# Kernel tuning notes

Hardware: AMD Instinct MI355X
Metric: run time of the kernel (lower is better)

The kernel has to match this reference:

```python
import jax, jax.numpy as jnp
import numpy as np

BETA = 0.25


def setup_inputs() -> dict:
    key = jax.random.key(0)
    k1, k2 = jax.random.split(key)
    z_e = jax.random.normal(k1, (16, 64, 64, 64), dtype=jnp.float32)  # (B, D, H, W)
    embedding = jax.random.normal(k2, (1024, 64), dtype=jnp.float32)  # (K, D)
    return {"z_e": z_e, "embedding": embedding}


def reference(z_e, embedding):
    B, D, H, W = z_e.shape
    # (B, D, H, W) -> (B, H, W, D) -> (N, D)
    flat = jnp.transpose(z_e, (0, 2, 3, 1)).reshape(-1, D)
    # squared L2 distances to codebook: (N, K)
    dist = (jnp.sum(flat * flat, axis=1, keepdims=True)
            + jnp.sum(embedding * embedding, axis=1)
            - 2.0 * flat @ embedding.T)
    indices = jnp.argmin(dist, axis=1)  # (N,)
    z_q_flat = embedding[indices]  # (N, D) gather
    z_q = jnp.transpose(z_q_flat.reshape(B, H, W, D), (0, 3, 1, 2))  # (B, D, H, W)
    codebook_loss = jnp.mean((jax.lax.stop_gradient(z_q) - z_e) ** 2)
    commit_loss = jnp.mean((z_q - jax.lax.stop_gradient(z_e)) ** 2)
    vq_loss = codebook_loss + BETA * commit_loss
    # straight-through estimator
    z_q_st = z_e + jax.lax.stop_gradient(z_q - z_e)
    return (z_q_st, vq_loss, indices.reshape(B, H, W))
```

## Files before the change

### kernel.cpp

```cpp
#include <hip/hip_runtime.h>
#include <math.h>

typedef short  short8 __attribute__((ext_vector_type(8)));
typedef float  f32x4  __attribute__((ext_vector_type(4)));

#define ZQ_ELEMS 4194304
#define KC       1024
#define EPS_HALF 0.005f


__device__ inline unsigned short bf16_rne(float f) {
    union { float fv; unsigned u; } a; a.fv = f;
    unsigned r = a.u + 0x7FFFu + ((a.u >> 16) & 1u);
    return (unsigned short)(r >> 16);
}
__device__ inline float bf16_to_f(unsigned short h) {
    union { unsigned u; float fv; } a; a.u = ((unsigned)h) << 16;
    return a.fv;
}
__device__ inline double dpack(float hi, unsigned lo) {
    return __hiloint2double(__float_as_int(hi), (int)lo);
}
__device__ inline float dhi(double d) { return __int_as_float(__double2hiint(d)); }
__device__ inline unsigned dlo(double d) { return (unsigned)__double2loint(d); }

__global__ __launch_bounds__(256) void vq_prep(const float* __restrict__ emb,
        unsigned short* __restrict__ epack, float* __restrict__ enorm,
        int* __restrict__ risky_cnt, float* __restrict__ out) {
    const int k = blockIdx.x * 256 + threadIdx.x;
    if (k == 0) { *risky_cnt = 0; out[ZQ_ELEMS] = 0.f; }
    const float4* e4 = (const float4*)(emb + k * 64);
    float s = 0.f;
#pragma unroll
    for (int j = 0; j < 16; ++j) {
        float4 v = e4[j];
        float vv[4] = {v.x, v.y, v.z, v.w};
        ushort4 hv, lv;
        unsigned short h[4], l[4];
#pragma unroll
        for (int t = 0; t < 4; ++t) {
            s = fmaf(vv[t], vv[t], s);
            h[t] = bf16_rne(vv[t]);
            l[t] = bf16_rne(vv[t] - bf16_to_f(h[t]));
        }
        hv.x = h[0]; hv.y = h[1]; hv.z = h[2]; hv.w = h[3];
        lv.x = l[0]; lv.y = l[1]; lv.z = l[2]; lv.w = l[3];
        *(ushort4*)(epack + k * 128 + j * 4)      = hv;
        *(ushort4*)(epack + k * 128 + 64 + j * 4) = lv;
    }
    enorm[k] = s;
}

__global__ __launch_bounds__(256) void vq_scan(const float* __restrict__ z_e,
        const unsigned short* __restrict__ epack, const float* __restrict__ enorm,
        const float* __restrict__ emb, float* __restrict__ out,
        int* __restrict__ risky_cnt, int* __restrict__ risky) {
    const int tid  = threadIdx.x;
    const int lane = tid & 63;
    const int col  = lane & 15;
    const int g    = lane >> 4;
    const int wv   = __builtin_amdgcn_readfirstlane(tid >> 6);
    const int pblk = blockIdx.x * 64;

    __shared__ __align__(16) char smem[19456];
    unsigned short* afrag = (unsigned short*)smem;
    double* mrgB = (double*)(smem + 16384);
    float*  mrgS = (float*)(smem + 18432);
    float (*zq)[65] = (float (*)[65])smem;
    __shared__ int   sidx[64];
    __shared__ float sred[4];

    {
        const int lp = tid & 63;
        const int pg = pblk + lp;
        const float* zb = z_e + (pg >> 12) * 262144 + (pg & 4095);
        const int sx = (lp & 7) << 3;
#pragma unroll
        for (int s8 = 0; s8 < 2; ++s8) {
            const int d0 = wv * 16 + s8 * 8;
            short8 H, L;
#pragma unroll
            for (int j = 0; j < 8; ++j) {
                float v = zb[(d0 + j) * 4096];
                unsigned short h = bf16_rne(v);
                H[j] = (short)h;
                L[j] = (short)bf16_rne(v - bf16_to_f(h));
            }
            const int sw = d0 ^ sx;
            *(short8*)&afrag[lp * 128 + sw]      = H;
            *(short8*)&afrag[lp * 128 + 64 + sw] = L;
        }
    }
    __syncthreads();

    const f32x4 zero4 = {0.f, 0.f, 0.f, 0.f};
    const int g8 = g * 8;

    double Brun[4];
    float  Srun[4];
#pragma unroll
    for (int it = 0; it < 4; ++it) { Brun[it] = dpack(-INFINITY, 0u); Srun[it] = -INFINITY; }

#pragma unroll 1
    for (int pass = 0; pass < 4; ++pass) {
        const int cbase = pass * 256 + wv * 64;
        short8 ah[4][2], al[4][2];
        f32x4 enf[4];
#pragma unroll
        for (int t = 0; t < 4; ++t) {
            const int code = cbase + t * 16 + col;
            const short8* ph = (const short8*)(epack + code * 128) + g;
            ah[t][0] = ph[0]; ah[t][1] = ph[4];
            al[t][0] = ph[8]; al[t][1] = ph[12];
            const float4 e4 = *(const float4*)(enorm + cbase + t * 16 + g * 4);
            enf[t][0] = -0.5f * e4.x; enf[t][1] = -0.5f * e4.y;
            enf[t][2] = -0.5f * e4.z; enf[t][3] = -0.5f * e4.w;
        }
        const int K1 = 1023 - cbase - g * 4;

#pragma unroll
        for (int it = 0; it < 4; ++it) {
            const int lpx = it * 16 + col;
            const int sxp = (lpx & 7) << 3;
            const unsigned short* ap = &afrag[lpx * 128];
            const short8 bh0 = *(const short8*)&ap[(g8     ) ^ sxp];
            const short8 bh1 = *(const short8*)&ap[(32 + g8) ^ sxp];
            const short8 bl0 = *(const short8*)&ap[64 + ((g8     ) ^ sxp)];
            const short8 bl1 = *(const short8*)&ap[64 + ((32 + g8) ^ sxp)];

            double cand[16];
#pragma unroll
            for (int t = 0; t < 4; ++t) {
                f32x4 aA, aB;
                aA = __builtin_amdgcn_mfma_f32_16x16x32_bf16(ah[t][0], bh0, enf[t], 0, 0, 0);
                aB = __builtin_amdgcn_mfma_f32_16x16x32_bf16(ah[t][1], bh1, zero4, 0, 0, 0);
                aA = __builtin_amdgcn_mfma_f32_16x16x32_bf16(al[t][0], bh0, aA, 0, 0, 0);
                aB = __builtin_amdgcn_mfma_f32_16x16x32_bf16(al[t][1], bh1, aB, 0, 0, 0);
                aA = __builtin_amdgcn_mfma_f32_16x16x32_bf16(ah[t][0], bl0, aA, 0, 0, 0);
                aB = __builtin_amdgcn_mfma_f32_16x16x32_bf16(ah[t][1], bl1, aB, 0, 0, 0);
#pragma unroll
                for (int r = 0; r < 4; ++r)
                    cand[t * 4 + r] = dpack(aA[r] + aB[r], (unsigned)(K1 - t * 16 - r));
            }
            double tB[8]; float tS[8];
#pragma unroll
            for (int i = 0; i < 8; ++i) {
                tB[i] = fmax(cand[2 * i], cand[2 * i + 1]);
                tS[i] = fminf(dhi(cand[2 * i]), dhi(cand[2 * i + 1]));
            }
#pragma unroll
            for (int lvl = 4; lvl >= 1; lvl >>= 1) {
#pragma unroll
                for (int i = 0; i < lvl; ++i) {
                    tS[i] = __builtin_amdgcn_fmed3f(dhi(tB[i]), dhi(tB[i + lvl]),
                                                    fmaxf(tS[i], tS[i + lvl]));
                    tB[i] = fmax(tB[i], tB[i + lvl]);
                }
            }
            Srun[it] = __builtin_amdgcn_fmed3f(dhi(Brun[it]), dhi(tB[0]),
                                               fmaxf(Srun[it], tS[0]));
            Brun[it] = fmax(Brun[it], tB[0]);
        }
    }

#pragma unroll
    for (int it = 0; it < 4; ++it) {
        double B = Brun[it];
        float  S = Srun[it];
#pragma unroll
        for (int s = 16; s < 64; s <<= 1) {
            const double ob = __shfl_xor(B, s, 64);
            const float  o2 = __shfl_xor(S, s, 64);
            S = __builtin_amdgcn_fmed3f(dhi(B), dhi(ob), fmaxf(S, o2));
            B = fmax(B, ob);
        }
        Brun[it] = B;
        Srun[it] = S;
    }
    __syncthreads();
    if (g == 0) {
#pragma unroll
        for (int it = 0; it < 4; ++it) {
            mrgB[wv * 64 + it * 16 + col] = Brun[it];
            mrgS[wv * 64 + it * 16 + col] = Srun[it];
        }
    }
    __syncthreads();

    if (tid < 64) {
        double B = mrgB[tid];
        float  S = mrgS[tid];
#pragma unroll
        for (int w = 1; w < 4; ++w) {
            const double ob = mrgB[w * 64 + tid];
            const float  o2 = mrgS[w * 64 + tid];
            S = __builtin_amdgcn_fmed3f(dhi(B), dhi(ob), fmaxf(S, o2));
            B = fmax(B, ob);
        }
        const int idx = 1023 - (int)dlo(B);
        sidx[tid] = idx;
        out[ZQ_ELEMS + 1 + pblk + tid] = (float)idx;
        const bool risk = (dhi(B) - S < EPS_HALF);
        const unsigned long long m = __ballot(risk);
        int base = 0;
        if (lane == 0 && m) base = atomicAdd(risky_cnt, __popcll(m));
        base = __shfl(base, 0, 64);
        if (risk) risky[base + __popcll(m & ((1ull << lane) - 1ull))] = pblk + tid;
    }
    __syncthreads();

#pragma unroll
    for (int i = 0; i < 16; ++i) {
        const int p = wv * 16 + i;
        const int k = sidx[p];
        zq[p][lane] = emb[k * 64 + lane];
    }
    __syncthreads();

    const int batch = pblk >> 12;
    const int hw0   = pblk & 4095;
    const int p4 = (tid & 15) * 4;
    const float* zeb = z_e + batch * 262144 + hw0;
    float* ob = out + batch * 262144 + hw0;
    float ss = 0.f;
#pragma unroll
    for (int it = 0; it < 4; ++it) {
        const int d = (tid >> 4) + it * 16;
        float4 q;
        q.x = zq[p4 + 0][d]; q.y = zq[p4 + 1][d];
        q.z = zq[p4 + 2][d]; q.w = zq[p4 + 3][d];
        const float4 z = *(const float4*)(zeb + d * 4096 + p4);
        *(float4*)(ob + d * 4096 + p4) = q;
        const float e0 = q.x - z.x, e1 = q.y - z.y, e2 = q.z - z.z, e3 = q.w - z.w;
        ss += e0 * e0 + e1 * e1 + e2 * e2 + e3 * e3;
    }
    for (int off = 32; off; off >>= 1) ss += __shfl_down(ss, off, 64);
    if (lane == 0) sred[wv] = ss;
    __syncthreads();
    if (tid == 0)
        atomicAdd(out + ZQ_ELEMS,
                  ((sred[0] + sred[1]) + (sred[2] + sred[3])) * (1.25f / (float)ZQ_ELEMS));
}

__global__ __launch_bounds__(256) void vq_fix(const float* __restrict__ z_e,
        const float* __restrict__ emb, float* __restrict__ out,
        const int* __restrict__ cnt, const int* __restrict__ list) {
    const int n = *cnt;
    if ((int)blockIdx.x * 4 >= n) return;
    __shared__ float etile[64][65];
    const int tid  = threadIdx.x;
    const int lane = tid & 63;
    const int wv   = __builtin_amdgcn_readfirstlane(tid >> 6);

    for (int base = blockIdx.x * 4; base < n; base += gridDim.x * 4) {
        const int item = base + wv;
        const bool active = item < n;
        int pix = 0, oldk = 0;
        float f[64];
        if (active) {
            pix = list[item];
            const float* zb = z_e + (pix >> 12) * 262144 + (pix & 4095);
#pragma unroll
            for (int d = 0; d < 64; ++d) f[d] = zb[d * 4096];
            oldk = (int)out[ZQ_ELEMS + 1 + pix];
        }
        double best = INFINITY; int bk = KC;
        double dold = 0.0;
        for (int j = 0; j < 16; ++j) {
            __syncthreads();
#pragma unroll
            for (int i = 0; i < 16; ++i) {
                const int idx = i * 256 + tid;
                etile[idx >> 6][idx & 63] = emb[j * 4096 + idx];
            }
            __syncthreads();
            if (active) {
                const int k = j * 64 + lane;
                double a0 = 0.0, a1 = 0.0;
#pragma unroll
                for (int d = 0; d < 64; d += 2) {
                    const double d0 = (double)f[d]     - (double)etile[lane][d];
                    const double d1 = (double)f[d + 1] - (double)etile[lane][d + 1];
                    a0 = fma(d0, d0, a0);
                    a1 = fma(d1, d1, a1);
                }
                const double acc = a0 + a1;
                if (acc < best || (acc == best && k < bk)) { best = acc; bk = k; }
                if (k == oldk) dold = acc;
            }
        }
        if (active) {
            for (int off = 32; off; off >>= 1) {
                const double ov = __shfl_down(best, off, 64);
                const int    oi = __shfl_down(bk, off, 64);
                if (ov < best || (ov == best && oi < bk)) { best = ov; bk = oi; }
            }
            for (int off = 32; off; off >>= 1) dold += __shfl_down(dold, off, 64);
            bk   = __shfl(bk, 0, 64);
            best = __shfl(best, 0, 64);
            dold = __shfl(dold, 0, 64);
            if (bk != oldk) {
                if (lane == 0) out[ZQ_ELEMS + 1 + pix] = (float)bk;
                out[(pix >> 12) * 262144 + (pix & 4095) + lane * 4096] = emb[bk * 64 + lane];
                if (lane == 0)
                    atomicAdd(out + ZQ_ELEMS,
                              (float)((best - dold) * (1.25 / (double)ZQ_ELEMS)));
            }
        }
    }
}

extern "C" void kernel_launch(void* const* d_in, const int* in_sizes, int n_in,
                              void* d_out, int out_size, void* d_ws, size_t ws_size,
                              hipStream_t stream) {
    const float* z_e = (const float*)d_in[0];
    const float* emb = (const float*)d_in[1];
    float* out = (float*)d_out;
    char* ws = (char*)d_ws;
    unsigned short* epack = (unsigned short*)ws;
    float*  enorm     = (float*)(ws + 262144);
    int*    risky_cnt = (int*)(ws + 266240);
    int*    risky     = (int*)(ws + 270336);

    vq_prep<<<4, 256, 0, stream>>>(emb, epack, enorm, risky_cnt, out);
    vq_scan<<<1024, 256, 0, stream>>>(z_e, epack, enorm, emb, out, risky_cnt, risky);
    vq_fix<<<512, 256, 0, stream>>>(z_e, emb, out, risky_cnt, risky);
}
```

Baseline: 78.95 us.

## Switch distance MFMA from 16x16x32 to 32x32x16 tiles with pre-scaled norms

Restructures the codebook scan to use 32x32x16 bf16 MFMA tiles. Each wave now covers 32 codes by 32 pixels per tile over 8 passes instead of 16x16 tiles over 4 passes. This cuts the number of MFMA issues and the cross-lane shuffle reduction, since the merge now needs one xor-32 step instead of two. The -0.5 scaling of the codebook norms moves into the prep kernel. The tradeoffs are larger accumulator register use and a different operand load pattern from global and LDS.

```diff
diff --git a/kernel.cpp b/kernel.cpp
--- a/kernel.cpp
+++ b/kernel.cpp
@@ -3,6 +3,7 @@
 
 typedef short  short8 __attribute__((ext_vector_type(8)));
 typedef float  f32x4  __attribute__((ext_vector_type(4)));
+typedef float  f32x16 __attribute__((ext_vector_type(16)));
 
 #define ZQ_ELEMS 4194304
 #define KC       1024
@@ -25,7 +26,7 @@
 __device__ inline unsigned dlo(double d) { return (unsigned)__double2loint(d); }
 
 __global__ __launch_bounds__(256) void vq_prep(const float* __restrict__ emb,
-        unsigned short* __restrict__ epack, float* __restrict__ enorm,
+        unsigned short* __restrict__ epack, float* __restrict__ enorm_s,
         int* __restrict__ risky_cnt, float* __restrict__ out) {
     const int k = blockIdx.x * 256 + threadIdx.x;
     if (k == 0) { *risky_cnt = 0; out[ZQ_ELEMS] = 0.f; }
@@ -48,17 +49,17 @@
         *(ushort4*)(epack + k * 128 + j * 4)      = hv;
         *(ushort4*)(epack + k * 128 + 64 + j * 4) = lv;
     }
-    enorm[k] = s;
+    enorm_s[k] = -0.5f * s;
 }
 
 __global__ __launch_bounds__(256) void vq_scan(const float* __restrict__ z_e,
-        const unsigned short* __restrict__ epack, const float* __restrict__ enorm,
+        const unsigned short* __restrict__ epack, const float* __restrict__ enorm_s,
         const float* __restrict__ emb, float* __restrict__ out,
         int* __restrict__ risky_cnt, int* __restrict__ risky) {
     const int tid  = threadIdx.x;
     const int lane = tid & 63;
-    const int col  = lane & 15;
-    const int g    = lane >> 4;
+    const int px   = lane & 31;
+    const int hi32 = lane >> 5;
     const int wv   = __builtin_amdgcn_readfirstlane(tid >> 6);
     const int pblk = blockIdx.x * 64;
 
@@ -93,55 +94,73 @@
     }
     __syncthreads();
 
-    const f32x4 zero4 = {0.f, 0.f, 0.f, 0.f};
-    const int g8 = g * 8;
-
-    double Brun[4];
-    float  Srun[4];
-#pragma unroll
-    for (int it = 0; it < 4; ++it) { Brun[it] = dpack(-INFINITY, 0u); Srun[it] = -INFINITY; }
+    const int half8 = hi32 * 8;
+    const f32x16 zero16 = {0.f,0.f,0.f,0.f,0.f,0.f,0.f,0.f,
+                           0.f,0.f,0.f,0.f,0.f,0.f,0.f,0.f};
+
+    double Brun[2];
+    float  Srun[2];
+#pragma unroll
+    for (int t = 0; t < 2; ++t) { Brun[t] = dpack(-INFINITY, 0u); Srun[t] = -INFINITY; }
 
 #pragma unroll 1
-    for (int pass = 0; pass < 4; ++pass) {
-        const int cbase = pass * 256 + wv * 64;
-        short8 ah[4][2], al[4][2];
-        f32x4 enf[4];
-#pragma unroll
-        for (int t = 0; t < 4; ++t) {
-            const int code = cbase + t * 16 + col;
-            const short8* ph = (const short8*)(epack + code * 128) + g;
-            ah[t][0] = ph[0]; ah[t][1] = ph[4];
-            al[t][0] = ph[8]; al[t][1] = ph[12];
-            const float4 e4 = *(const float4*)(enorm + cbase + t * 16 + g * 4);
-            enf[t][0] = -0.5f * e4.x; enf[t][1] = -0.5f * e4.y;
-            enf[t][2] = -0.5f * e4.z; enf[t][3] = -0.5f * e4.w;
-        }
-        const int K1 = 1023 - cbase - g * 4;
-
-#pragma unroll
-        for (int it = 0; it < 4; ++it) {
-            const int lpx = it * 16 + col;
+    for (int pass = 0; pass < 8; ++pass) {
+        const int cbase = pass * 128 + wv * 32;
+        const unsigned short* pe = epack + (cbase + px) * 128 + half8;
+        const short8 ah0 = *(const short8*)(pe);
+        const short8 ah1 = *(const short8*)(pe + 16);
+        const short8 ah2 = *(const short8*)(pe + 32);
+        const short8 ah3 = *(const short8*)(pe + 48);
+        const short8 al0 = *(const short8*)(pe + 64);
+        const short8 al1 = *(const short8*)(pe + 80);
+        const short8 al2 = *(const short8*)(pe + 96);
+        const short8 al3 = *(const short8*)(pe + 112);
+        f32x16 enf;
+        {
+            const float4 e0 = *(const float4*)(enorm_s + cbase + 4 * hi32);
+            const float4 e1 = *(const float4*)(enorm_s + cbase + 4 * hi32 + 8);
+            const float4 e2 = *(const float4*)(enorm_s + cbase + 4 * hi32 + 16);
+            const float4 e3 = *(const float4*)(enorm_s + cbase + 4 * hi32 + 24);
+            enf[0]=e0.x; enf[1]=e0.y; enf[2]=e0.z; enf[3]=e0.w;
+            enf[4]=e1.x; enf[5]=e1.y; enf[6]=e1.z; enf[7]=e1.w;
+            enf[8]=e2.x; enf[9]=e2.y; enf[10]=e2.z; enf[11]=e2.w;
+            enf[12]=e3.x; enf[13]=e3.y; enf[14]=e3.z; enf[15]=e3.w;
+        }
+        const int K1 = 1023 - cbase - 4 * hi32;
+
+#pragma unroll
+        for (int tile = 0; tile < 2; ++tile) {
+            const int lpx = tile * 32 + px;
             const int sxp = (lpx & 7) << 3;
-            const unsigned short* ap = &afrag[lpx * 128];
-            const short8 bh0 = *(const short8*)&ap[(g8     ) ^ sxp];
-            const short8 bh1 = *(const short8*)&ap[(32 + g8) ^ sxp];
-            const short8 bl0 = *(const short8*)&ap[64 + ((g8     ) ^ sxp)];
-            const short8 bl1 = *(const short8*)&ap[64 + ((32 + g8) ^ sxp)];
+            const unsigned short* bp = &afrag[lpx * 128];
+            const short8 bh0 = *(const short8*)&bp[(0  + half8) ^ sxp];
+            const short8 bh1 = *(const short8*)&bp[(16 + half8) ^ sxp];
+            const short8 bh2 = *(const short8*)&bp[(32 + half8) ^ sxp];
+            const short8 bh3 = *(const short8*)&bp[(48 + half8) ^ sxp];
+            const short8 bl0 = *(const short8*)&bp[64 + ((0  + half8) ^ sxp)];
+            const short8 bl1 = *(const short8*)&bp[64 + ((16 + half8) ^ sxp)];
+            const short8 bl2 = *(const short8*)&bp[64 + ((32 + half8) ^ sxp)];
+            const short8 bl3 = *(const short8*)&bp[64 + ((48 + half8) ^ sxp)];
+
+            f32x16 aA = enf, aB = zero16;
+            aA = __builtin_amdgcn_mfma_f32_32x32x16_bf16(ah0, bh0, aA, 0, 0, 0);
+            aB = __builtin_amdgcn_mfma_f32_32x32x16_bf16(ah2, bh2, aB, 0, 0, 0);
+            aA = __builtin_amdgcn_mfma_f32_32x32x16_bf16(al0, bh0, aA, 0, 0, 0);
+            aB = __builtin_amdgcn_mfma_f32_32x32x16_bf16(al2, bh2, aB, 0, 0, 0);
+            aA = __builtin_amdgcn_mfma_f32_32x32x16_bf16(ah0, bl0, aA, 0, 0, 0);
+            aB = __builtin_amdgcn_mfma_f32_32x32x16_bf16(ah2, bl2, aB, 0, 0, 0);
+            aA = __builtin_amdgcn_mfma_f32_32x32x16_bf16(ah1, bh1, aA, 0, 0, 0);
+            aB = __builtin_amdgcn_mfma_f32_32x32x16_bf16(ah3, bh3, aB, 0, 0, 0);
+            aA = __builtin_amdgcn_mfma_f32_32x32x16_bf16(al1, bh1, aA, 0, 0, 0);
+            aB = __builtin_amdgcn_mfma_f32_32x32x16_bf16(al3, bh3, aB, 0, 0, 0);
+            aA = __builtin_amdgcn_mfma_f32_32x32x16_bf16(ah1, bl1, aA, 0, 0, 0);
+            aB = __builtin_amdgcn_mfma_f32_32x32x16_bf16(ah3, bl3, aB, 0, 0, 0);
 
             double cand[16];
 #pragma unroll
-            for (int t = 0; t < 4; ++t) {
-                f32x4 aA, aB;
-                aA = __builtin_amdgcn_mfma_f32_16x16x32_bf16(ah[t][0], bh0, enf[t], 0, 0, 0);
-                aB = __builtin_amdgcn_mfma_f32_16x16x32_bf16(ah[t][1], bh1, zero4, 0, 0, 0);
-                aA = __builtin_amdgcn_mfma_f32_16x16x32_bf16(al[t][0], bh0, aA, 0, 0, 0);
-                aB = __builtin_amdgcn_mfma_f32_16x16x32_bf16(al[t][1], bh1, aB, 0, 0, 0);
-                aA = __builtin_amdgcn_mfma_f32_16x16x32_bf16(ah[t][0], bl0, aA, 0, 0, 0);
-                aB = __builtin_amdgcn_mfma_f32_16x16x32_bf16(ah[t][1], bl1, aB, 0, 0, 0);
-#pragma unroll
-                for (int r = 0; r < 4; ++r)
-                    cand[t * 4 + r] = dpack(aA[r] + aB[r], (unsigned)(K1 - t * 16 - r));
-            }
+            for (int reg = 0; reg < 16; ++reg)
+                cand[reg] = dpack(aA[reg] + aB[reg],
+                                  (unsigned)(K1 - (reg & 3) - 8 * (reg >> 2)));
             double tB[8]; float tS[8];
 #pragma unroll
             for (int i = 0; i < 8; ++i) {
@@ -157,34 +176,22 @@
                     tB[i] = fmax(tB[i], tB[i + lvl]);
                 }
             }
-            Srun[it] = __builtin_amdgcn_fmed3f(dhi(Brun[it]), dhi(tB[0]),
-                                               fmaxf(Srun[it], tS[0]));
-            Brun[it] = fmax(Brun[it], tB[0]);
-        }
-    }
-
-#pragma unroll
-    for (int it = 0; it < 4; ++it) {
-        double B = Brun[it];
-        float  S = Srun[it];
-#pragma unroll
-        for (int s = 16; s < 64; s <<= 1) {
-            const double ob = __shfl_xor(B, s, 64);
-            const float  o2 = __shfl_xor(S, s, 64);
-            S = __builtin_amdgcn_fmed3f(dhi(B), dhi(ob), fmaxf(S, o2));
-            B = fmax(B, ob);
-        }
-        Brun[it] = B;
-        Srun[it] = S;
-    }
-    __syncthreads();
-    if (g == 0) {
-#pragma unroll
-        for (int it = 0; it < 4; ++it) {
-            mrgB[wv * 64 + it * 16 + col] = Brun[it];
-            mrgS[wv * 64 + it * 16 + col] = Srun[it];
-        }
-    }
+            Srun[tile] = __builtin_amdgcn_fmed3f(dhi(Brun[tile]), dhi(tB[0]),
+                                                 fmaxf(Srun[tile], tS[0]));
+            Brun[tile] = fmax(Brun[tile], tB[0]);
+        }
+    }
+
+#pragma unroll
+    for (int t = 0; t < 2; ++t) {
+        const double ob = __shfl_xor(Brun[t], 32, 64);
+        const float  o2 = __shfl_xor(Srun[t], 32, 64);
+        Srun[t] = __builtin_amdgcn_fmed3f(dhi(Brun[t]), dhi(ob), fmaxf(Srun[t], o2));
+        Brun[t] = fmax(Brun[t], ob);
+    }
+    __syncthreads();
+    mrgB[wv * 64 + lane] = hi32 ? Brun[1] : Brun[0];
+    mrgS[wv * 64 + lane] = hi32 ? Srun[1] : Srun[0];
     __syncthreads();
 
     if (tid < 64) {
@@ -318,11 +325,11 @@
     float* out = (float*)d_out;
     char* ws = (char*)d_ws;
     unsigned short* epack = (unsigned short*)ws;
-    float*  enorm     = (float*)(ws + 262144);
+    float*  enorm_s   = (float*)(ws + 262144);
     int*    risky_cnt = (int*)(ws + 266240);
     int*    risky     = (int*)(ws + 270336);
 
-    vq_prep<<<4, 256, 0, stream>>>(emb, epack, enorm, risky_cnt, out);
-    vq_scan<<<1024, 256, 0, stream>>>(z_e, epack, enorm, emb, out, risky_cnt, risky);
+    vq_prep<<<4, 256, 0, stream>>>(emb, epack, enorm_s, risky_cnt, out);
+    vq_scan<<<1024, 256, 0, stream>>>(z_e, epack, enorm_s, emb, out, risky_cnt, risky);
     vq_fix<<<512, 256, 0, stream>>>(z_e, emb, out, risky_cnt, risky);
 }
```

After: 80.55 us (median of 2 runs). +2.0%, slower.
